# Kernel optimization log

Measured on AMD Instinct MI355X. Metric: run time of the kernel, lower is better.

The kernel has to match this reference:

```python
import jax, jax.numpy as jnp
import numpy as np

HEADS1, HID1 = 4, 64   # layer 1: concat -> 256
HEADS2, HID2 = 1, 64   # layer 2: out_channels
NEG_SLOPE = 0.2


def gat_layer(x_src, x_dst, W_src, W_dst, att_src, att_dst, bias, src, dst, n_tgt, heads, hid):
    # bipartite GATConv (PyG math), concat heads
    xs = (x_src @ W_src).reshape(-1, heads, hid)          # [Ns,H,C]
    xd = (x_dst @ W_dst).reshape(-1, heads, hid)          # [Nt,H,C]
    a_s = jnp.sum(xs * att_src, axis=-1)                  # [Ns,H]
    a_d = jnp.sum(xd * att_dst, axis=-1)                  # [Nt,H]
    e = jax.nn.leaky_relu(a_s[src] + a_d[dst], NEG_SLOPE) # [E,H]
    m = jax.ops.segment_max(e, dst, num_segments=n_tgt)
    m = jnp.where(jnp.isfinite(m), m, 0.0)
    ex = jnp.exp(e - m[dst])
    denom = jax.ops.segment_sum(ex, dst, num_segments=n_tgt)
    alpha = ex / (denom[dst] + 1e-16)                     # edge softmax per target
    msg = xs[src] * alpha[:, :, None]                     # [E,H,C]
    out = jax.ops.segment_sum(msg, dst, num_segments=n_tgt)
    return out.reshape(n_tgt, heads * hid) + bias


def setup_inputs() -> dict:
    key = jax.random.key(0)
    ks = jax.random.split(key, 20)
    N0, NT1, NT2 = 100000, 25000, 5000
    E1, E2 = 400000, 100000
    IN, H1 = 256, HEADS1 * HID1  # 256
    OUT = HEADS2 * HID2          # 64
    g = lambda k, sh, fan: jax.random.normal(k, sh, jnp.float32) * (1.0 / np.sqrt(fan))
    return {
        'x': jax.random.normal(ks[0], (N0, IN), jnp.float32),
        'src1': jax.random.randint(ks[1], (E1,), 0, N0),
        'dst1': jax.random.randint(ks[2], (E1,), 0, NT1),
        'src2': jax.random.randint(ks[3], (E2,), 0, NT1),
        'dst2': jax.random.randint(ks[4], (E2,), 0, NT2),
        'n_tgt1': NT1, 'n_tgt2': NT2,
        'W1_src': g(ks[5], (IN, H1), IN), 'W1_dst': g(ks[6], (IN, H1), IN),
        'att1_src': g(ks[7], (HEADS1, HID1), HID1), 'att1_dst': g(ks[8], (HEADS1, HID1), HID1),
        'bias1': jnp.zeros((H1,), jnp.float32),
        'skip1_W': g(ks[9], (IN, H1), IN), 'skip1_b': jnp.zeros((H1,), jnp.float32),
        'W2_src': g(ks[10], (H1, OUT), H1), 'W2_dst': g(ks[11], (H1, OUT), H1),
        'att2_src': g(ks[12], (HEADS2, HID2), HID2), 'att2_dst': g(ks[13], (HEADS2, HID2), HID2),
        'bias2': jnp.zeros((OUT,), jnp.float32),
        'skip2_W': g(ks[14], (H1, OUT), H1), 'skip2_b': jnp.zeros((OUT,), jnp.float32),
    }


def reference(x, src1, dst1, src2, dst2, n_tgt1, n_tgt2,
              W1_src, W1_dst, att1_src, att1_dst, bias1, skip1_W, skip1_b,
              W2_src, W2_dst, att2_src, att2_dst, bias2, skip2_W, skip2_b):
    # layer 1: conv + skip + elu (dropout inactive in eval)
    x_t1 = x[:n_tgt1]
    h = gat_layer(x, x_t1, W1_src, W1_dst, att1_src, att1_dst, bias1,
                  src1, dst1, n_tgt1, HEADS1, HID1)
    h = h + (x_t1 @ skip1_W + skip1_b)
    h = jax.nn.elu(h)
    # layer 2 (final): conv + skip, then log_softmax
    x_t2 = h[:n_tgt2]
    o = gat_layer(h, x_t2, W2_src, W2_dst, att2_src, att2_dst, bias2,
                  src2, dst2, n_tgt2, HEADS2, HID2)
    o = o + (x_t2 @ skip2_W + skip2_b)
    return jax.nn.log_softmax(o, axis=-1)
```

## Files before the change

kernel.cpp:

```cpp
#include <hip/hip_runtime.h>
#include <hip/hip_bf16.h>

using bf16 = __hip_bfloat16;
typedef __attribute__((ext_vector_type(8))) short short8;
typedef __attribute__((ext_vector_type(4))) short short4v;
typedef __attribute__((ext_vector_type(4))) float float4v;

__device__ __forceinline__ short f2bs(float x) {
    bf16 b = __float2bfloat16(x);
    return __builtin_bit_cast(short, b);
}
__device__ __forceinline__ float bs2f(short s) {
    return __uint_as_float(((unsigned)(unsigned short)s) << 16);
}
__device__ __forceinline__ void glds16(const void* g, void* l) {
    __builtin_amdgcn_global_load_lds(
        (const __attribute__((address_space(1))) unsigned int*)g,
        (__attribute__((address_space(3))) unsigned int*)l, 16, 0, 0);
}

__global__ __launch_bounds__(512, 4) void gemm_l1(
        const bf16* __restrict__ A, const bf16* __restrict__ Bt,
        bf16* __restrict__ xs1, bf16* __restrict__ sk1,
        float* __restrict__ as1, float* __restrict__ ad1,
        const float* __restrict__ att_s, const float* __restrict__ att_d,
        int M, int NT) {
    __shared__ short ldsB[32 * 512];
    const int y = blockIdx.x;
    const int row0 = blockIdx.y * 128;
    if (y >= 4 && row0 >= NT) return;
    const int col0 = y * 64;
    const int tid = threadIdx.x;
    const int wave = tid >> 6, lane = tid & 63;
    const int quad = lane >> 4, l16 = lane & 15;

#pragma unroll
    for (int i = 0; i < 4; i++) {
        int blk = wave * 4 + i;
        int cb = blk >> 3, kit = blk & 7;
        glds16(&Bt[(size_t)(col0 + cb * 16 + l16) * 256 + kit * 32 + quad * 8],
               &ldsB[blk * 512]);
    }

    const int arow_ = row0 + wave * 16 + l16;
    const int arow = arow_ < M ? arow_ : M - 1;
    const bf16* Ap = &A[(size_t)arow * 256 + quad * 8];

    short8 s[8];
#pragma unroll
    for (int kit = 0; kit < 8; kit++) s[kit] = *(const short8*)(Ap + kit * 32);

    const float4v fz = {0.f, 0.f, 0.f, 0.f};
    float4v acc[4];
#pragma unroll
    for (int n = 0; n < 4; n++) acc[n] = fz;

    __syncthreads();

#pragma unroll
    for (int kit = 0; kit < 8; kit++) {
#pragma unroll
        for (int n = 0; n < 4; n++) {
            short8 bf = *(short8*)&ldsB[(n * 8 + kit) * 512 + lane * 8];
            acc[n] = __builtin_amdgcn_mfma_f32_16x16x32_bf16(s[kit], bf, acc[n], 0, 0, 0);
        }
    }

    const int rbase = row0 + wave * 16 + quad * 4;

    if (y < 8) {
        const float* attc = y < 4 ? att_s : att_d;
        const int head = y & 3;
        const int aM = y < 4 ? M : NT;
        float* aout = y < 4 ? as1 : ad1;
        float av[4];
#pragma unroll
        for (int n = 0; n < 4; n++) av[n] = attc[head * 64 + n * 16 + l16];
#pragma unroll
        for (int r = 0; r < 4; r++) {
            float t = acc[0][r] * av[0] + acc[1][r] * av[1] +
                      acc[2][r] * av[2] + acc[3][r] * av[3];
            t += __shfl_xor(t, 1, 64);
            t += __shfl_xor(t, 2, 64);
            t += __shfl_xor(t, 4, 64);
            t += __shfl_xor(t, 8, 64);
            int grow = rbase + r;
            if (l16 == 0 && grow < aM) aout[(size_t)grow * 4 + head] = t;
        }
    }

    if (y < 4) {
#pragma unroll
        for (int n = 0; n < 4; n++) {
            int col = col0 + n * 16 + l16;
#pragma unroll
            for (int r = 0; r < 4; r++) {
                int row = rbase + r;
                if (row < M) xs1[(size_t)row * 256 + col] = __float2bfloat16(acc[n][r]);
            }
        }
    } else if (y >= 8) {
#pragma unroll
        for (int n = 0; n < 4; n++) {
            int scol = col0 - 512 + n * 16 + l16;
#pragma unroll
            for (int r = 0; r < 4; r++) {
                int row = rbase + r;
                if (row < NT) sk1[(size_t)row * 256 + scol] = __float2bfloat16(acc[n][r]);
            }
        }
    }
}

__global__ __launch_bounds__(512, 4) void gemm_l2(
        const bf16* __restrict__ Ah, const bf16* __restrict__ Bt,
        float* __restrict__ x2, float* __restrict__ a2,
        const float* __restrict__ attc, int NT) {
    __shared__ short ldsB[32 * 512];
    const int y = blockIdx.y;
    const int row0 = blockIdx.x * 128;
    const int col0 = y * 64;
    const int tid = threadIdx.x;
    const int wave = tid >> 6, lane = tid & 63;
    const int quad = lane >> 4, l16 = lane & 15;

#pragma unroll
    for (int i = 0; i < 4; i++) {
        int blk = wave * 4 + i;
        int cb = blk >> 3, kit = blk & 7;
        glds16(&Bt[(size_t)(col0 + cb * 16 + l16) * 256 + kit * 32 + quad * 8],
               &ldsB[blk * 512]);
    }

    const int arow = row0 + wave * 16 + l16;
    const bf16* Ap = &Ah[(size_t)arow * 256 + quad * 8];

    short8 s[8];
#pragma unroll
    for (int kit = 0; kit < 8; kit++) s[kit] = *(const short8*)(Ap + kit * 32);

    const float4v fz = {0.f, 0.f, 0.f, 0.f};
    float4v acc[4];
#pragma unroll
    for (int n = 0; n < 4; n++) acc[n] = fz;

    __syncthreads();

#pragma unroll
    for (int kit = 0; kit < 8; kit++) {
#pragma unroll
        for (int n = 0; n < 4; n++) {
            short8 bf = *(short8*)&ldsB[(n * 8 + kit) * 512 + lane * 8];
            acc[n] = __builtin_amdgcn_mfma_f32_16x16x32_bf16(s[kit], bf, acc[n], 0, 0, 0);
        }
    }

    const int rbase = row0 + wave * 16 + quad * 4;

    if (y < 2) {
        float av[4];
#pragma unroll
        for (int n = 0; n < 4; n++) av[n] = attc[y * 64 + n * 16 + l16];
#pragma unroll
        for (int r = 0; r < 4; r++) {
            float t = acc[0][r] * av[0] + acc[1][r] * av[1] +
                      acc[2][r] * av[2] + acc[3][r] * av[3];
            t += __shfl_xor(t, 1, 64);
            t += __shfl_xor(t, 2, 64);
            t += __shfl_xor(t, 4, 64);
            t += __shfl_xor(t, 8, 64);
            int grow = rbase + r;
            if (l16 == 0 && grow < NT) a2[(size_t)grow * 2 + y] = t;
        }
    }
#pragma unroll
    for (int n = 0; n < 4; n++) {
        int col = col0 + n * 16 + l16;
#pragma unroll
        for (int r = 0; r < 4; r++) {
            int row = rbase + r;
            if (row < NT) x2[(size_t)row * 192 + col] = acc[n][r];
        }
    }
}

__global__ void prep_fused(
        const int* __restrict__ s1, const int* __restrict__ d1, int E1,
        const int* __restrict__ s2, const int* __restrict__ d2, int E2,
        int* __restrict__ fill1, int* __restrict__ fill2,
        int* __restrict__ psrc1, int* __restrict__ psrc2,
        const float* __restrict__ x, bf16* __restrict__ xbf, int N0,
        const float* __restrict__ W1s, const float* __restrict__ W1d,
        const float* __restrict__ W1sk, const float* __restrict__ W2s,
        const float* __restrict__ W2d, const float* __restrict__ W2sk,
        const float* __restrict__ a2s, const float* __restrict__ a2d,
        bf16* __restrict__ Wt1, bf16* __restrict__ Wt2,
        float* __restrict__ at2c) {
    int t = blockIdx.x * blockDim.x + threadIdx.x;
    if (t < E1) {
        int d = d1[t];
        int pos = atomicAdd(&fill1[d], 1);
        if (pos < 64) psrc1[(d << 6) + pos] = s1[t];
        return;
    }
    t -= E1;
    if (t < E2) {
        int d = d2[t];
        int pos = atomicAdd(&fill2[d], 1);
        if (pos < 64) psrc2[(d << 6) + pos] = s2[t];
        return;
    }
    t -= E2;
    const int NC = N0 * 32;
    if (t < NC) {
        const float4v* p = (const float4v*)&x[(size_t)t * 8];
        float4v a = p[0], b = p[1];
        short8 v;
#pragma unroll
        for (int j = 0; j < 4; j++) { v[j] = f2bs(a[j]); v[4 + j] = f2bs(b[j]); }
        *(short8*)&xbf[(size_t)t * 8] = v;
        return;
    }
    t -= NC;
    if (t < 196608) {
        int n = t >> 8, k = t & 255;
        const float* W = n < 256 ? W1s : (n < 512 ? W1d : W1sk);
        Wt1[t] = __float2bfloat16(W[k * 256 + (n & 255)]);
    } else if (t < 245760) {
        int i = t - 196608;
        int n = i >> 8, k = i & 255;
        const float* W = n < 64 ? W2s : (n < 128 ? W2d : W2sk);
        Wt2[i] = __float2bfloat16(W[k * 64 + (n & 63)]);
    } else if (t < 245888) {
        int i = t - 245760;
        at2c[i] = i < 64 ? a2s[i] : a2d[i - 64];
    }
}

__global__ __launch_bounds__(256) void agg_h4(
        const int* __restrict__ fill, const int* __restrict__ psrc,
        const bf16* __restrict__ X, const float* __restrict__ as1,
        const float* __restrict__ ad1, const float* __restrict__ bias,
        const bf16* __restrict__ skip, const float* __restrict__ skipb,
        bf16* __restrict__ h) {
    __shared__ float exl[4][64][4];
    __shared__ float red[4][256];
    const int d = blockIdx.x;
    const int tid = threadIdx.x;
    const int wv = tid >> 6, lane = tid & 63;
    const int head = lane >> 4;
    int deg = fill[d];
    deg = deg < 64 ? deg : 64;
    int se = 0;
    float4v ex4 = {0.f, 0.f, 0.f, 0.f};
    const float4v ad4 = *(const float4v*)&ad1[(size_t)d * 4];
    if (lane < deg) {
        se = psrc[((size_t)d << 6) + lane];
        float4v as4 = *(const float4v*)&as1[(size_t)se * 4];
#pragma unroll
        for (int c = 0; c < 4; c++) {
            float v = as4[c] + ad4[c];
            v = v > 0.f ? v : 0.2f * v;
            ex4[c] = expf(v);
        }
    }
    *(float4v*)&exl[wv][lane][0] = ex4;
    float4v dn = ex4;
#pragma unroll
    for (int o = 32; o; o >>= 1) {
        dn.x += __shfl_xor(dn.x, o, 64);
        dn.y += __shfl_xor(dn.y, o, 64);
        dn.z += __shfl_xor(dn.z, o, 64);
        dn.w += __shfl_xor(dn.w, o, 64);
    }
    float4v acc = {0.f, 0.f, 0.f, 0.f}, acc2 = {0.f, 0.f, 0.f, 0.f};
    int p = wv;
    for (; p + 4 < deg; p += 8) {
        int sA = __shfl(se, p, 64), sB = __shfl(se, p + 4, 64);
        float aA = exl[wv][p][head], aB = exl[wv][p + 4][head];
        short4v xa = *(const short4v*)&X[(size_t)sA * 256 + lane * 4];
        short4v xb = *(const short4v*)&X[(size_t)sB * 256 + lane * 4];
        acc.x += bs2f(xa.x) * aA; acc2.x += bs2f(xb.x) * aB;
        acc.y += bs2f(xa.y) * aA; acc2.y += bs2f(xb.y) * aB;
        acc.z += bs2f(xa.z) * aA; acc2.z += bs2f(xb.z) * aB;
        acc.w += bs2f(xa.w) * aA; acc2.w += bs2f(xb.w) * aB;
    }
    for (; p < deg; p += 4) {
        int sA = __shfl(se, p, 64);
        float aA = exl[wv][p][head];
        short4v xa = *(const short4v*)&X[(size_t)sA * 256 + lane * 4];
        acc.x += bs2f(xa.x) * aA;
        acc.y += bs2f(xa.y) * aA;
        acc.z += bs2f(xa.z) * aA;
        acc.w += bs2f(xa.w) * aA;
    }
    acc.x += acc2.x; acc.y += acc2.y; acc.z += acc2.z; acc.w += acc2.w;
    *(float4v*)&red[wv][lane * 4] = acc;
    __syncthreads();
    const int f = tid;
    float sum = red[0][f] + red[1][f] + red[2][f] + red[3][f];
    int hf = f >> 6;
    float den = hf == 0 ? dn.x : hf == 1 ? dn.y : hf == 2 ? dn.z : dn.w;
    float v = sum / (den + 1e-16f) + bias[f] + __bfloat162float(skip[(size_t)d * 256 + f]) +
              skipb[f];
    h[(size_t)d * 256 + f] = __float2bfloat16(v > 0.f ? v : expm1f(v));
}

__global__ __launch_bounds__(256) void agg_h1(
        const int* __restrict__ fill2, const int* __restrict__ psrc2,
        const float* __restrict__ x2, const float* __restrict__ a2,
        const float* __restrict__ bias, const float* __restrict__ skipb,
        float* __restrict__ out, int M) {
    const int d = blockIdx.x * 4 + (threadIdx.x >> 6);
    const int lane = threadIdx.x & 63;
    if (d >= M) return;
    int deg = fill2[d];
    deg = deg < 64 ? deg : 64;
    int se = 0;
    float exv = 0.f;
    const float adv = a2[(size_t)d * 2 + 1];
    if (lane < deg) {
        se = psrc2[((size_t)d << 6) + lane];
        float v = a2[(size_t)se * 2] + adv;
        v = v > 0.f ? v : 0.2f * v;
        exv = expf(v);
    }
    float den = exv;
#pragma unroll
    for (int o = 32; o; o >>= 1) den += __shfl_xor(den, o, 64);
    float acc = 0.f, acc2 = 0.f;
    int p = 0;
    for (; p + 1 < deg; p += 2) {
        int sA = __shfl(se, p, 64), sB = __shfl(se, p + 1, 64);
        float aA = __shfl(exv, p, 64), aB = __shfl(exv, p + 1, 64);
        acc += x2[(size_t)sA * 192 + lane] * aA;
        acc2 += x2[(size_t)sB * 192 + lane] * aB;
    }
    if (p < deg) {
        int sA = __shfl(se, p, 64);
        acc += x2[(size_t)sA * 192 + lane] * __shfl(exv, p, 64);
    }
    float v = (acc + acc2) / (den + 1e-16f) + bias[lane] +
              x2[(size_t)d * 192 + 128 + lane] + skipb[lane];
    float m = v;
#pragma unroll
    for (int o = 32; o; o >>= 1) m = fmaxf(m, __shfl_xor(m, o, 64));
    float e = expf(v - m);
#pragma unroll
    for (int o = 32; o; o >>= 1) e += __shfl_xor(e, o, 64);
    out[(size_t)d * 64 + lane] = v - m - logf(e);
}

extern "C" void kernel_launch(void* const* d_in, const int* in_sizes, int n_in,
                              void* d_out, int out_size, void* d_ws, size_t ws_size,
                              hipStream_t stream) {
    const float* x        = (const float*)d_in[0];
    const int*   src1     = (const int*)d_in[1];
    const int*   dst1     = (const int*)d_in[2];
    const int*   src2     = (const int*)d_in[3];
    const int*   dst2     = (const int*)d_in[4];
    const float* W1_src   = (const float*)d_in[7];
    const float* W1_dst   = (const float*)d_in[8];
    const float* att1_src = (const float*)d_in[9];
    const float* att1_dst = (const float*)d_in[10];
    const float* bias1    = (const float*)d_in[11];
    const float* skip1_W  = (const float*)d_in[12];
    const float* skip1_b  = (const float*)d_in[13];
    const float* W2_src   = (const float*)d_in[14];
    const float* W2_dst   = (const float*)d_in[15];
    const float* att2_src = (const float*)d_in[16];
    const float* att2_dst = (const float*)d_in[17];
    const float* bias2    = (const float*)d_in[18];
    const float* skip2_W  = (const float*)d_in[19];
    const float* skip2_b  = (const float*)d_in[20];

    const int N0  = in_sizes[0] / 256;
    const int E1  = in_sizes[1];
    const int E2  = in_sizes[3];
    const int NT1 = 25000, NT2 = 5000;
    const int NT1p = 25088;

    char* ws = (char*)d_ws;
    size_t off = 0;
    auto alloc = [&](size_t b) { size_t o = off; off += (b + 255) & ~(size_t)255; return o; };
    size_t o_xbf   = alloc((size_t)N0 * 256 * 2);
    size_t o_xs1   = alloc((size_t)N0 * 256 * 2);
    size_t o_sk1   = alloc((size_t)NT1 * 256 * 2);
    size_t o_h     = alloc((size_t)NT1p * 256 * 2);
    size_t o_as1   = alloc((size_t)N0 * 4 * 4);
    size_t o_ad1   = alloc((size_t)NT1 * 4 * 4);
    size_t o_fill  = alloc((size_t)(NT1 + NT2) * 4);
    size_t o_psrc1 = alloc((size_t)NT1 * 64 * 4);
    size_t o_psrc2 = alloc((size_t)NT2 * 64 * 4);
    size_t o_wt1   = alloc((size_t)768 * 256 * 2);
    size_t o_wt2   = alloc((size_t)192 * 256 * 2);
    size_t o_at2c  = alloc((size_t)128 * 4);
    size_t off2a = o_xs1;
    auto alloc2 = [&](size_t b) { size_t o = off2a; off2a += (b + 255) & ~(size_t)255; return o; };
    size_t o_x2 = alloc2((size_t)NT1 * 192 * 4);
    size_t o_a2 = alloc2((size_t)NT1 * 2 * 4);

    bf16*  xbf   = (bf16*)(ws + o_xbf);
    bf16*  xs1   = (bf16*)(ws + o_xs1);
    bf16*  sk1   = (bf16*)(ws + o_sk1);
    bf16*  h     = (bf16*)(ws + o_h);
    float* as1   = (float*)(ws + o_as1);
    float* ad1   = (float*)(ws + o_ad1);
    int*   fill1 = (int*)(ws + o_fill);
    int*   fill2 = fill1 + NT1;
    int*   psrc1 = (int*)(ws + o_psrc1);
    int*   psrc2 = (int*)(ws + o_psrc2);
    bf16*  Wt1   = (bf16*)(ws + o_wt1);
    bf16*  Wt2   = (bf16*)(ws + o_wt2);
    float* at2c  = (float*)(ws + o_at2c);
    float* x2    = (float*)(ws + o_x2);
    float* a2    = (float*)(ws + o_a2);

    hipMemsetAsync(fill1, 0, (size_t)(NT1 + NT2) * 4, stream);
    {
        int total = E1 + E2 + N0 * 32 + 245888;
        prep_fused<<<(total + 255) / 256, 256, 0, stream>>>(
            src1, dst1, E1, src2, dst2, E2, fill1, fill2, psrc1, psrc2,
            x, xbf, N0, W1_src, W1_dst, skip1_W, W2_src, W2_dst, skip2_W,
            att2_src, att2_dst, Wt1, Wt2, at2c);
    }
    gemm_l1<<<dim3(12, (N0 + 127) / 128), 512, 0, stream>>>(
        xbf, Wt1, xs1, sk1, as1, ad1, att1_src, att1_dst, N0, NT1);
    agg_h4<<<NT1, 256, 0, stream>>>(fill1, psrc1, xs1, as1, ad1, bias1, sk1, skip1_b, h);
    gemm_l2<<<dim3((NT1 + 127) / 128, 3), 512, 0, stream>>>(h, Wt2, x2, a2, at2c, NT1);
    agg_h1<<<(NT2 + 3) / 4, 256, 0, stream>>>(fill2, psrc2, x2, a2, bias2, skip2_b,
                                              (float*)d_out, NT2);
}
```

Before: 354.3 us.

## Fuse fp32-to-bf16 input conversion into layer-1 GEMM and loop all column tiles per block

Removes the separate pass that converted the 100k×256 fp32 input to a bf16 workspace copy. The layer-1 GEMM now loads fp32 rows, converts them to bf16 fragments in registers once, and reuses them across all 12 (or 4) column tiles within a single block. B tiles are double-buffered in LDS so the next tile is staged while the current one is computed. This removes a full write and re-read of the converted input, but it lowers grid parallelism, doubles LDS per block, and serialises the column tiles inside each block.

```diff
diff --git a/kernel.cpp b/kernel.cpp
--- a/kernel.cpp
+++ b/kernel.cpp
@@ -20,95 +20,113 @@
 }
 
 __global__ __launch_bounds__(512, 4) void gemm_l1(
-        const bf16* __restrict__ A, const bf16* __restrict__ Bt,
+        const float* __restrict__ A, const bf16* __restrict__ Bt,
         bf16* __restrict__ xs1, bf16* __restrict__ sk1,
         float* __restrict__ as1, float* __restrict__ ad1,
         const float* __restrict__ att_s, const float* __restrict__ att_d,
         int M, int NT) {
-    __shared__ short ldsB[32 * 512];
-    const int y = blockIdx.x;
-    const int row0 = blockIdx.y * 128;
-    if (y >= 4 && row0 >= NT) return;
-    const int col0 = y * 64;
+    __shared__ short ldsB[2][32 * 512];
+    const int row0 = blockIdx.x * 128;
     const int tid = threadIdx.x;
     const int wave = tid >> 6, lane = tid & 63;
     const int quad = lane >> 4, l16 = lane & 15;
 
-#pragma unroll
-    for (int i = 0; i < 4; i++) {
-        int blk = wave * 4 + i;
-        int cb = blk >> 3, kit = blk & 7;
-        glds16(&Bt[(size_t)(col0 + cb * 16 + l16) * 256 + kit * 32 + quad * 8],
-               &ldsB[blk * 512]);
-    }
+    auto stageB = [&](int y, int buf) {
+#pragma unroll
+        for (int i = 0; i < 4; i++) {
+            int blk = wave * 4 + i;
+            int cb = blk >> 3, kit = blk & 7;
+            glds16(&Bt[(size_t)(y * 64 + cb * 16 + l16) * 256 + kit * 32 + quad * 8],
+                   &ldsB[buf][blk * 512]);
+        }
+    };
+
+    stageB(0, 0);
 
     const int arow_ = row0 + wave * 16 + l16;
     const int arow = arow_ < M ? arow_ : M - 1;
-    const bf16* Ap = &A[(size_t)arow * 256 + quad * 8];
-
-    short8 s[8];
-#pragma unroll
-    for (int kit = 0; kit < 8; kit++) s[kit] = *(const short8*)(Ap + kit * 32);
-
-    const float4v fz = {0.f, 0.f, 0.f, 0.f};
-    float4v acc[4];
-#pragma unroll
-    for (int n = 0; n < 4; n++) acc[n] = fz;
+    const float* Ap = &A[(size_t)arow * 256 + quad * 8];
+    short8 afr[8];
+#pragma unroll
+    for (int half = 0; half < 2; half++) {
+        float4v r0[4], r1[4];
+#pragma unroll
+        for (int k = 0; k < 4; k++) {
+            r0[k] = *(const float4v*)(Ap + (half * 4 + k) * 32);
+            r1[k] = *(const float4v*)(Ap + (half * 4 + k) * 32 + 4);
+        }
+#pragma unroll
+        for (int k = 0; k < 4; k++) {
+            short8 v;
+#pragma unroll
+            for (int j = 0; j < 4; j++) { v[j] = f2bs(r0[k][j]); v[4 + j] = f2bs(r1[k][j]); }
+            afr[half * 4 + k] = v;
+        }
+    }
+
+    const int ymax = row0 < NT ? 12 : 4;
+    const int rbase = row0 + wave * 16 + quad * 4;
 
     __syncthreads();
 
-#pragma unroll
-    for (int kit = 0; kit < 8; kit++) {
-#pragma unroll
-        for (int n = 0; n < 4; n++) {
-            short8 bf = *(short8*)&ldsB[(n * 8 + kit) * 512 + lane * 8];
-            acc[n] = __builtin_amdgcn_mfma_f32_16x16x32_bf16(s[kit], bf, acc[n], 0, 0, 0);
-        }
-    }
-
-    const int rbase = row0 + wave * 16 + quad * 4;
-
-    if (y < 8) {
-        const float* attc = y < 4 ? att_s : att_d;
-        const int head = y & 3;
-        const int aM = y < 4 ? M : NT;
-        float* aout = y < 4 ? as1 : ad1;
-        float av[4];
-#pragma unroll
-        for (int n = 0; n < 4; n++) av[n] = attc[head * 64 + n * 16 + l16];
-#pragma unroll
-        for (int r = 0; r < 4; r++) {
-            float t = acc[0][r] * av[0] + acc[1][r] * av[1] +
-                      acc[2][r] * av[2] + acc[3][r] * av[3];
-            t += __shfl_xor(t, 1, 64);
-            t += __shfl_xor(t, 2, 64);
-            t += __shfl_xor(t, 4, 64);
-            t += __shfl_xor(t, 8, 64);
-            int grow = rbase + r;
-            if (l16 == 0 && grow < aM) aout[(size_t)grow * 4 + head] = t;
-        }
-    }
-
-    if (y < 4) {
-#pragma unroll
-        for (int n = 0; n < 4; n++) {
-            int col = col0 + n * 16 + l16;
+    for (int y = 0; y < ymax; y++) {
+        const int cur = y & 1;
+        if (y + 1 < ymax) stageB(y + 1, cur ^ 1);
+
+        const float4v fz = {0.f, 0.f, 0.f, 0.f};
+        float4v acc[4];
+#pragma unroll
+        for (int n = 0; n < 4; n++) acc[n] = fz;
+#pragma unroll
+        for (int kit = 0; kit < 8; kit++)
+#pragma unroll
+            for (int n = 0; n < 4; n++) {
+                short8 bf = *(short8*)&ldsB[cur][(n * 8 + kit) * 512 + lane * 8];
+                acc[n] = __builtin_amdgcn_mfma_f32_16x16x32_bf16(afr[kit], bf, acc[n], 0, 0, 0);
+            }
+
+        if (y < 8) {
+            const float* attc = y < 4 ? att_s : att_d;
+            const int head = y & 3;
+            const int aM = y < 4 ? M : NT;
+            float* aout = y < 4 ? as1 : ad1;
+            float av[4];
+#pragma unroll
+            for (int n = 0; n < 4; n++) av[n] = attc[head * 64 + n * 16 + l16];
 #pragma unroll
             for (int r = 0; r < 4; r++) {
-                int row = rbase + r;
-                if (row < M) xs1[(size_t)row * 256 + col] = __float2bfloat16(acc[n][r]);
+                float t = acc[0][r] * av[0] + acc[1][r] * av[1] +
+                          acc[2][r] * av[2] + acc[3][r] * av[3];
+                t += __shfl_xor(t, 1, 64);
+                t += __shfl_xor(t, 2, 64);
+                t += __shfl_xor(t, 4, 64);
+                t += __shfl_xor(t, 8, 64);
+                int grow = rbase + r;
+                if (l16 == 0 && grow < aM) aout[(size_t)grow * 4 + head] = t;
             }
         }
-    } else if (y >= 8) {
-#pragma unroll
-        for (int n = 0; n < 4; n++) {
-            int scol = col0 - 512 + n * 16 + l16;
-#pragma unroll
-            for (int r = 0; r < 4; r++) {
-                int row = rbase + r;
-                if (row < NT) sk1[(size_t)row * 256 + scol] = __float2bfloat16(acc[n][r]);
+        if (y < 4) {
+#pragma unroll
+            for (int n = 0; n < 4; n++) {
+                int col = y * 64 + n * 16 + l16;
+#pragma unroll
+                for (int r = 0; r < 4; r++) {
+                    int row = rbase + r;
+                    if (row < M) xs1[(size_t)row * 256 + col] = __float2bfloat16(acc[n][r]);
+                }
             }
-        }
+        } else if (y >= 8) {
+#pragma unroll
+            for (int n = 0; n < 4; n++) {
+                int scol = (y - 8) * 64 + n * 16 + l16;
+#pragma unroll
+                for (int r = 0; r < 4; r++) {
+                    int row = rbase + r;
+                    if (row < NT) sk1[(size_t)row * 256 + scol] = __float2bfloat16(acc[n][r]);
+                }
+            }
+        }
+        __syncthreads();
     }
 }
 
@@ -184,12 +202,11 @@
     }
 }
 
-__global__ void prep_fused(
+__global__ void prep_s(
         const int* __restrict__ s1, const int* __restrict__ d1, int E1,
         const int* __restrict__ s2, const int* __restrict__ d2, int E2,
         int* __restrict__ fill1, int* __restrict__ fill2,
         int* __restrict__ psrc1, int* __restrict__ psrc2,
-        const float* __restrict__ x, bf16* __restrict__ xbf, int N0,
         const float* __restrict__ W1s, const float* __restrict__ W1d,
         const float* __restrict__ W1sk, const float* __restrict__ W2s,
         const float* __restrict__ W2d, const float* __restrict__ W2sk,
@@ -211,17 +228,6 @@
         return;
     }
     t -= E2;
-    const int NC = N0 * 32;
-    if (t < NC) {
-        const float4v* p = (const float4v*)&x[(size_t)t * 8];
-        float4v a = p[0], b = p[1];
-        short8 v;
-#pragma unroll
-        for (int j = 0; j < 4; j++) { v[j] = f2bs(a[j]); v[4 + j] = f2bs(b[j]); }
-        *(short8*)&xbf[(size_t)t * 8] = v;
-        return;
-    }
-    t -= NC;
     if (t < 196608) {
         int n = t >> 8, k = t & 255;
         const float* W = n < 256 ? W1s : (n < 512 ? W1d : W1sk);
@@ -371,8 +377,8 @@
     const float* att2_src = (const float*)d_in[16];
     const float* att2_dst = (const float*)d_in[17];
     const float* bias2    = (const float*)d_in[18];
+    const float* skip2_b  = (const float*)d_in[20];
     const float* skip2_W  = (const float*)d_in[19];
-    const float* skip2_b  = (const float*)d_in[20];
 
     const int N0  = in_sizes[0] / 256;
     const int E1  = in_sizes[1];
@@ -383,7 +389,6 @@
     char* ws = (char*)d_ws;
     size_t off = 0;
     auto alloc = [&](size_t b) { size_t o = off; off += (b + 255) & ~(size_t)255; return o; };
-    size_t o_xbf   = alloc((size_t)N0 * 256 * 2);
     size_t o_xs1   = alloc((size_t)N0 * 256 * 2);
     size_t o_sk1   = alloc((size_t)NT1 * 256 * 2);
     size_t o_h     = alloc((size_t)NT1p * 256 * 2);
@@ -400,7 +405,6 @@
     size_t o_x2 = alloc2((size_t)NT1 * 192 * 4);
     size_t o_a2 = alloc2((size_t)NT1 * 2 * 4);
 
-    bf16*  xbf   = (bf16*)(ws + o_xbf);
     bf16*  xs1   = (bf16*)(ws + o_xs1);
     bf16*  sk1   = (bf16*)(ws + o_sk1);
     bf16*  h     = (bf16*)(ws + o_h);
@@ -418,14 +422,14 @@
 
     hipMemsetAsync(fill1, 0, (size_t)(NT1 + NT2) * 4, stream);
     {
-        int total = E1 + E2 + N0 * 32 + 245888;
-        prep_fused<<<(total + 255) / 256, 256, 0, stream>>>(
+        int total = E1 + E2 + 245888;
+        prep_s<<<(total + 255) / 256, 256, 0, stream>>>(
             src1, dst1, E1, src2, dst2, E2, fill1, fill2, psrc1, psrc2,
-            x, xbf, N0, W1_src, W1_dst, skip1_W, W2_src, W2_dst, skip2_W,
+            W1_src, W1_dst, skip1_W, W2_src, W2_dst, skip2_W,
             att2_src, att2_dst, Wt1, Wt2, at2c);
     }
-    gemm_l1<<<dim3(12, (N0 + 127) / 128), 512, 0, stream>>>(
-        xbf, Wt1, xs1, sk1, as1, ad1, att1_src, att1_dst, N0, NT1);
+    gemm_l1<<<(N0 + 127) / 128, 512, 0, stream>>>(
+        x, Wt1, xs1, sk1, as1, ad1, att1_src, att1_dst, N0, NT1);
     agg_h4<<<NT1, 256, 0, stream>>>(fill1, psrc1, xs1, as1, ad1, bias1, sk1, skip1_b, h);
     gemm_l2<<<dim3((NT1 + 127) / 128, 3), 512, 0, stream>>>(h, Wt2, x2, a2, at2c, NT1);
     agg_h1<<<(NT2 + 3) / 4, 256, 0, stream>>>(fill2, psrc2, x2, a2, bias2, skip2_b,
```

After: 326.4 us. 7.9% less time.
